# Performance work log

Measured on AMD Instinct MI355X. Metric: run time of the kernel, lower is better.

Reference implementation:

```python
import jax, jax.numpy as jnp
import numpy as np

N = 50000          # nodes
E = 800000         # edges (before self-loops)
IN_CH = 16
HID = 32
HEADS = 4
NEG_SLOPE = 0.2    # PyG GATConv default leaky_relu slope


def add_self_loops(edge_index, n):
    loops = jnp.arange(n, dtype=edge_index.dtype)
    return jnp.concatenate([edge_index, jnp.stack([loops, loops])], axis=1)


def gat_layer(x, edge_index, W, a_src, a_dst, bias, heads, out_ch, concat):
    """PyG-style GATConv: gather -> attention logits -> segment softmax over dst -> scatter."""
    n = x.shape[0]
    h = (x @ W).reshape(n, heads, out_ch)            # [N, H, C]
    src, dst = edge_index[0], edge_index[1]          # messages flow src -> dst
    alpha_src = (h * a_src).sum(-1)                  # [N, H]
    alpha_dst = (h * a_dst).sum(-1)                  # [N, H]
    e = jax.nn.leaky_relu(alpha_src[src] + alpha_dst[dst], NEG_SLOPE)  # [Etot, H]
    # numerically stable segment softmax over incoming edges of each dst node
    e_max = jax.ops.segment_max(e, dst, num_segments=n)
    e_exp = jnp.exp(e - e_max[dst])
    denom = jax.ops.segment_sum(e_exp, dst, num_segments=n)
    alpha = e_exp / (denom[dst] + 1e-16)             # [Etot, H]
    out = jax.ops.segment_sum(h[src] * alpha[..., None], dst, num_segments=n)  # [N, H, C]
    out = out.reshape(n, heads * out_ch) if concat else out.mean(axis=1)
    return out + bias


def setup_inputs() -> dict:
    key = jax.random.key(0)
    ks = jax.random.split(key, 10)
    x = jax.random.normal(ks[0], (N, IN_CH), dtype=jnp.float32)
    edge_index = jax.random.randint(ks[1], (2, E), 0, N, dtype=jnp.int64)
    s = 0.1
    W1 = jax.random.normal(ks[2], (IN_CH, HEADS * HID), dtype=jnp.float32) * s
    a_src1 = jax.random.normal(ks[3], (1, HEADS, HID), dtype=jnp.float32) * s
    a_dst1 = jax.random.normal(ks[4], (1, HEADS, HID), dtype=jnp.float32) * s
    b1 = jnp.zeros((HEADS * HID,), dtype=jnp.float32)
    W2 = jax.random.normal(ks[5], (HEADS * HID, 2), dtype=jnp.float32) * s
    a_src2 = jax.random.normal(ks[6], (1, 1, 2), dtype=jnp.float32) * s
    a_dst2 = jax.random.normal(ks[7], (1, 1, 2), dtype=jnp.float32) * s
    b2 = jnp.zeros((2,), dtype=jnp.float32)
    return {"x": x, "edge_index": edge_index,
            "W1": W1, "a_src1": a_src1, "a_dst1": a_dst1, "b1": b1,
            "W2": W2, "a_src2": a_src2, "a_dst2": a_dst2, "b2": b2}


def reference(x, edge_index, W1, a_src1, a_dst1, b1, W2, a_src2, a_dst2, b2):
    ei = add_self_loops(edge_index, x.shape[0])
    h = gat_layer(x, ei, W1, a_src1, a_dst1, b1, HEADS, HID, concat=True)
    h = jax.nn.relu(h)
    out = gat_layer(h, ei, W2, a_src2, a_dst2, b2, 1, 2, concat=False)
    return out
```

## Files before the change

kernel.cpp:

```cpp
#include <hip/hip_runtime.h>
#include <hip/hip_bf16.h>

#define N_NODES 50000
#define N_EDGES 800000
#define ETOT    (N_EDGES + N_NODES)
#define STRIDE  64
#define IN_CH   16
#define HID     32
#define HEADS   4
#define C1      (HEADS * HID)
#define NEG     0.2f

#define DEG_BLOCKS ((ETOT / 4 + 255) / 256)
#define NGROUPS    (N_NODES / 4)
#define H1_BLOCKS  2048

typedef unsigned short u16;
typedef unsigned int   u32;

__device__ __forceinline__ float bf2f(u16 b) {
    return __uint_as_float(((u32)b) << 16);
}

__device__ __forceinline__ u16 f2bf(float f) {
    __hip_bfloat16 hb = __float2bfloat16(f);
    return *(u16*)&hb;
}

__device__ __forceinline__ int clampn(int v) {
    return v < 0 ? 0 : (v >= N_NODES ? N_NODES - 1 : v);
}

__device__ __forceinline__ int eidx(const int* ei, int e, int i64, int which) {
    int v = i64 ? ei[2 * (which * N_EDGES + e)] : ei[which * N_EDGES + e];
    return clampn(v);
}

__device__ __forceinline__ float cvt(const void* src, int i, int bf) {
    return bf ? bf2f(((const u16*)src)[i]) : ((const float*)src)[i];
}

__device__ __forceinline__ int probe_bf_wave(const u16* xb) {
    int l = threadIdx.x & 63;
    int my = 0;
#pragma unroll
    for (int k = 0; k < 4; k++) {
        float f = bf2f(xb[l * 4 + k]);
        float a = fabsf(f);
        if (f == 0.0f || (a > 9.5e-7f && a < 1.05e6f)) my++;
    }
#pragma unroll
    for (int m = 32; m; m >>= 1) my += __shfl_xor(my, m);
    return my >= 224;
}

__device__ __forceinline__ int probe_i64_wave(const int* ei32) {
    int l = threadIdx.x & 63;
    int nz = (l < 32 && ei32[2 * l + 1] != 0) ? 1 : 0;
#pragma unroll
    for (int m = 32; m; m >>= 1) nz += __shfl_xor(nz, m);
    return nz == 0;
}

__device__ __forceinline__ void dev_deg(const int* __restrict__ ei,
                                        int* __restrict__ degs,
                                        u32* __restrict__ srp, int blk) {
    int i64 = probe_i64_wave(ei);
    int e0 = (blk * 256 + (int)threadIdx.x) * 4;
    if (e0 >= ETOT) return;
    int s[4], d[4];
#pragma unroll
    for (int j = 0; j < 4; j++) {
        int e = e0 + j;
        if (e < N_EDGES) { s[j] = eidx(ei, e, i64, 0); d[j] = eidx(ei, e, i64, 1); }
        else             { s[j] = d[j] = e - N_EDGES; }
    }
    u32 r[4];
#pragma unroll
    for (int j = 0; j < 4; j++) {
        u32 rr = (u32)atomicAdd(&degs[d[j]], 1) + 1u;
        r[j] = ((u32)s[j] << 16) | (rr > 0xFFFFu ? 0xFFFFu : rr);
    }
    *(uint4*)(srp + e0) = make_uint4(r[0], r[1], r[2], r[3]);
}

__device__ __forceinline__ void dev_fill(const int* __restrict__ ei,
                                         const u32* __restrict__ srp,
                                         u16* __restrict__ csr, int blk) {
    int i64 = probe_i64_wave(ei);
    int e0 = (blk * 256 + (int)threadIdx.x) * 4;
    if (e0 >= ETOT) return;
    uint4 q = *(const uint4*)(srp + e0);
    u32 sr[4] = {q.x, q.y, q.z, q.w};
#pragma unroll
    for (int j = 0; j < 4; j++) {
        int e = e0 + j;
        int d = (e < N_EDGES) ? eidx(ei, e, i64, 1) : (e - N_EDGES);
        u32 r = sr[j] & 0xFFFFu;
        if (r < STRIDE) csr[d * STRIDE + r] = (u16)(sr[j] >> 16);
    }
}

__device__ __forceinline__ void dev_h1(const void* __restrict__ x,
                                       const void* __restrict__ W1,
                                       const void* __restrict__ a_s,
                                       const void* __restrict__ a_d,
                                       u32* __restrict__ h1u,
                                       float* __restrict__ as1,
                                       float* __restrict__ ad1,
                                       float* Ws, float* As, float* Ad, int blk) {
    int bf = probe_bf_wave((const u16*)x);
    if (blk == 0 && threadIdx.x < 4) as1[N_NODES * 4 + threadIdx.x] = -1e30f;
    if (bf) {
        const u32* w32 = (const u32*)W1;
        for (int i = threadIdx.x; i < IN_CH * C1 / 2; i += 256) {
            u32 v = w32[i];
            Ws[2 * i]     = bf2f((u16)(v & 0xFFFF));
            Ws[2 * i + 1] = bf2f((u16)(v >> 16));
        }
        const u32* s32 = (const u32*)a_s;
        const u32* d32 = (const u32*)a_d;
        for (int i = threadIdx.x; i < C1 / 2; i += 256) {
            u32 vs = s32[i], vd = d32[i];
            As[2 * i]     = bf2f((u16)(vs & 0xFFFF));
            As[2 * i + 1] = bf2f((u16)(vs >> 16));
            Ad[2 * i]     = bf2f((u16)(vd & 0xFFFF));
            Ad[2 * i + 1] = bf2f((u16)(vd >> 16));
        }
    } else {
        for (int i = threadIdx.x; i < IN_CH * C1; i += 256) Ws[i] = ((const float*)W1)[i];
        for (int i = threadIdx.x; i < C1; i += 256) {
            As[i] = ((const float*)a_s)[i];
            Ad[i] = ((const float*)a_d)[i];
        }
    }
    __syncthreads();

    int w = threadIdx.x >> 6, l = threadIdx.x & 63;
    int c0 = 2 * l, c1 = 2 * l + 1;
    for (int g = blk; g < NGROUPS; g += H1_BLOCKS) {
        int n = g * 4 + w;
        float xval = (l < IN_CH) ? cvt(x, n * IN_CH + l, bf) : 0.f;
        float acc0 = 0.f, acc1 = 0.f;
#pragma unroll
        for (int k = 0; k < IN_CH; k++) {
            float xk = __shfl(xval, k);
            acc0 += xk * Ws[k * C1 + c0];
            acc1 += xk * Ws[k * C1 + c1];
        }
        h1u[n * 64 + l] = (u32)f2bf(acc0) | ((u32)f2bf(acc1) << 16);

        float ps = acc0 * As[c0] + acc1 * As[c1];
        float pd = acc0 * Ad[c0] + acc1 * Ad[c1];
#pragma unroll
        for (int m = 8; m; m >>= 1) { ps += __shfl_xor(ps, m); pd += __shfl_xor(pd, m); }
        if ((l & 15) == 0) {
            int hd = l >> 4;
            as1[n * 4 + hd] = ps;
            ad1[n * 4 + hd] = pd;
        }
    }
}

__launch_bounds__(256)
__global__ void k_deg_h1(const void* __restrict__ x, const int* __restrict__ ei,
                         const void* __restrict__ W1, const void* __restrict__ a_s,
                         const void* __restrict__ a_d,
                         int* __restrict__ degs, u32* __restrict__ srp,
                         u32* __restrict__ h1u, float* __restrict__ as1,
                         float* __restrict__ ad1) {
    __shared__ float Ws[IN_CH * C1];
    __shared__ float As[C1], Ad[C1];
    if (blockIdx.x < DEG_BLOCKS) { dev_deg(ei, degs, srp, blockIdx.x); return; }
    dev_h1(x, W1, a_s, a_d, h1u, as1, ad1, Ws, As, Ad, blockIdx.x - DEG_BLOCKS);
}

__launch_bounds__(256)
__global__ void k_deg(const int* __restrict__ ei, int* __restrict__ degs,
                      u32* __restrict__ srp) {
    dev_deg(ei, degs, srp, blockIdx.x);
}

__launch_bounds__(256)
__global__ void k_fill(const int* __restrict__ ei, const u32* __restrict__ srp,
                       u16* __restrict__ csr) {
    dev_fill(ei, srp, csr, blockIdx.x);
}

__launch_bounds__(256)
__global__ void k_h1_only(const void* __restrict__ x, const void* __restrict__ W1,
                          const void* __restrict__ a_s, const void* __restrict__ a_d,
                          u32* __restrict__ h1u, float* __restrict__ as1,
                          float* __restrict__ ad1) {
    __shared__ float Ws[IN_CH * C1];
    __shared__ float As[C1], Ad[C1];
    dev_h1(x, W1, a_s, a_d, h1u, as1, ad1, Ws, As, Ad, blockIdx.x);
}

__launch_bounds__(256)
__global__ void k_gather1(const void* __restrict__ x,
                          const int* __restrict__ degs, const u16* __restrict__ csr,
                          const u32* __restrict__ h1u,
                          const float* __restrict__ as1, const float* __restrict__ ad1,
                          const void* __restrict__ b1, const void* __restrict__ W2,
                          const void* __restrict__ a2s, const void* __restrict__ a2d,
                          float* __restrict__ h2, float* __restrict__ as2,
                          float* __restrict__ ad2) {
    int bf = probe_bf_wave((const u16*)x);
    int n = blockIdx.x * 4 + (threadIdx.x >> 6);
    int l = threadIdx.x & 63;
    int hd = l >> 4;
    int je = l & 7;
    int jh = (l >> 3) & 3;
    float advb = ad1[n * 4 + jh];
    int deg = degs[n] + 1;
    deg = deg > STRIDE ? STRIDE : deg;
    int nb = (deg + 7) >> 3;
    const u16* row = csr + (size_t)n * STRIDE;
    float acc0 = 0.f, acc1 = 0.f, swd = 0.f;

    int se = (int)row[je];
    if (se >= N_NODES) se = N_NODES;
    for (int b = 0; b < nb; b++) {
        int se_next = 0xFFFF;
        if (b + 1 < nb) se_next = (int)row[(b + 1) * 8 + je];
        float t = as1[se * 4 + jh] + advb;
        t = t > 0.f ? t : NEG * t;
        float wm = __expf(t);
        swd += wm;
#pragma unroll
        for (int j = 0; j < 8; j++) {
            int   sj = __shfl(se, j);
            float wj = __shfl(wm, hd * 8 + j);
            u32 p = h1u[sj * 64 + l];
            acc0 += wj * bf2f((u16)(p & 0xFFFF));
            acc1 += wj * bf2f((u16)(p >> 16));
        }
        se = se_next >= N_NODES ? N_NODES : se_next;
    }

    swd += __shfl_xor(swd, 1);
    swd += __shfl_xor(swd, 2);
    swd += __shfl_xor(swd, 4);
    float sw = __shfl(swd, hd * 8);

    float inv = 1.0f / sw;
    float v0 = acc0 * inv + cvt(b1, 2 * l, bf);
    float v1 = acc1 * inv + cvt(b1, 2 * l + 1, bf);
    v0 = v0 > 0.f ? v0 : 0.f;
    v1 = v1 > 0.f ? v1 : 0.f;
    float p0 = v0 * cvt(W2, 4 * l,     bf) + v1 * cvt(W2, 4 * l + 2, bf);
    float p1 = v0 * cvt(W2, 4 * l + 1, bf) + v1 * cvt(W2, 4 * l + 3, bf);
#pragma unroll
    for (int d = 32; d; d >>= 1) { p0 += __shfl_down(p0, d); p1 += __shfl_down(p1, d); }
    if (l == 0) {
        h2[n * 2] = p0; h2[n * 2 + 1] = p1;
        as2[n] = p0 * cvt(a2s, 0, bf) + p1 * cvt(a2s, 1, bf);
        ad2[n] = p0 * cvt(a2d, 0, bf) + p1 * cvt(a2d, 1, bf);
    }
}

__launch_bounds__(256)
__global__ void k_gather2(const void* __restrict__ x,
                          const int* __restrict__ degs, const u16* __restrict__ csr,
                          const float* __restrict__ h2, const float* __restrict__ as2,
                          const float* __restrict__ ad2, const void* __restrict__ b2,
                          void* __restrict__ out) {
    int bf = probe_bf_wave((const u16*)x);
    int n = blockIdx.x * 16 + (threadIdx.x >> 4);
    int g = threadIdx.x & 15;
    float adv = ad2[n], a0 = 0.f, a1 = 0.f, sw = 0.f;
    int deg = degs[n] + 1;
    deg = deg > STRIDE ? STRIDE : deg;
    const u16* row = csr + (size_t)n * STRIDE;
    for (int k = g; k < deg; k += 16) {
        int s = (int)row[k];
        float lg = as2[s] + adv;
        lg = lg > 0.f ? lg : NEG * lg;
        float w = __expf(lg);
        float2 hv = ((const float2*)h2)[s];
        a0 += w * hv.x;
        a1 += w * hv.y;
        sw += w;
    }
#pragma unroll
    for (int m = 8; m; m >>= 1) {
        a0 += __shfl_xor(a0, m); a1 += __shfl_xor(a1, m); sw += __shfl_xor(sw, m);
    }
    if (g == 0) {
        float inv = 1.0f / sw;
        float o0 = a0 * inv + cvt(b2, 0, bf);
        float o1 = a1 * inv + cvt(b2, 1, bf);
        if (bf) {
            ((u32*)out)[n] = (u32)f2bf(o0) | ((u32)f2bf(o1) << 16);
        } else {
            ((float2*)out)[n] = make_float2(o0, o1);
        }
    }
}

extern "C" void kernel_launch(void* const* d_in, const int* in_sizes, int n_in,
                              void* d_out, int out_size, void* d_ws, size_t ws_size,
                              hipStream_t stream) {
    const void* x    = d_in[0];
    const int*  ei   = (const int*)d_in[1];
    const void* W1   = d_in[2];
    const void* a_s1 = d_in[3];
    const void* a_d1 = d_in[4];
    const void* b1   = d_in[5];
    const void* W2   = d_in[6];
    const void* a_s2 = d_in[7];
    const void* a_d2 = d_in[8];
    const void* b2   = d_in[9];

    char* p = (char*)d_ws;
    int*   degs = (int*)p;     p += ((size_t)N_NODES * 4 + 255) & ~255;
    u16*   csr  = (u16*)p;     p += (size_t)N_NODES * STRIDE * 2;
    size_t init_bytes = (size_t)(p - (char*)d_ws);
    u32*   h1u  = (u32*)p;     p += (size_t)(N_NODES + 1) * 64 * 4;
    float* as1  = (float*)p;   p += (size_t)(N_NODES + 1) * HEADS * 4;
    float* ad1  = (float*)p;   p += (size_t)N_NODES * HEADS * 4;
    float* h2   = (float*)p;   p += (size_t)N_NODES * 2 * 4;
    float* as2  = (float*)p;   p += (size_t)N_NODES * 4;
    float* ad2  = (float*)p;   p += (size_t)N_NODES * 4;
    size_t base_used = (size_t)(p - (char*)d_ws);
    size_t srp_bytes = (size_t)ETOT * 4;

    hipMemsetAsync(degs, 0xFF, init_bytes, stream);

    if (ws_size >= base_used + srp_bytes) {
        u32* srp = (u32*)p;
        k_deg_h1<<<DEG_BLOCKS + H1_BLOCKS, 256, 0, stream>>>(
            x, ei, W1, a_s1, a_d1, degs, srp, h1u, as1, ad1);
        k_fill<<<DEG_BLOCKS, 256, 0, stream>>>(ei, srp, csr);
    } else {
        u32* srp = h1u;
        k_deg<<<DEG_BLOCKS, 256, 0, stream>>>(ei, degs, srp);
        k_fill<<<DEG_BLOCKS, 256, 0, stream>>>(ei, srp, csr);
        k_h1_only<<<H1_BLOCKS, 256, 0, stream>>>(x, W1, a_s1, a_d1, h1u, as1, ad1);
    }
    k_gather1<<<N_NODES / 4, 256, 0, stream>>>(
        x, degs, csr, h1u, as1, ad1, b1, W2, a_s2, a_d2, h2, as2, ad2);
    k_gather2<<<N_NODES / 16, 256, 0, stream>>>(
        x, degs, csr, h2, as2, ad2, b2, d_out);
}
```

Baseline: 204.2 us.

## Fuse degree count and CSR fill, keep layer-1 weights in registers

Merges the degree-counting and CSR-fill passes into one. Each edge's atomicAdd return value now writes the source index straight into its slot of the padded CSR, which removes the intermediate srp buffer, one kernel launch and a second read of edge_index. The h1 projection now loads W1 and the attention vectors into per-lane registers and reads each node's x row with vector loads. That drops the shared-memory staging, the __syncthreads and the per-k shuffles, at the cost of higher register use. The workspace-size fallback path is removed, and the padding row of h1u is zeroed explicitly.

```diff
diff --git a/kernel.cpp b/kernel.cpp
--- a/kernel.cpp
+++ b/kernel.cpp
@@ -62,9 +62,9 @@
     return nz == 0;
 }
 
-__device__ __forceinline__ void dev_deg(const int* __restrict__ ei,
-                                        int* __restrict__ degs,
-                                        u32* __restrict__ srp, int blk) {
+__device__ __forceinline__ void dev_degfill(const int* __restrict__ ei,
+                                            int* __restrict__ degs,
+                                            u16* __restrict__ csr, int blk) {
     int i64 = probe_i64_wave(ei);
     int e0 = (blk * 256 + (int)threadIdx.x) * 4;
     if (e0 >= ETOT) return;
@@ -75,29 +75,10 @@
         if (e < N_EDGES) { s[j] = eidx(ei, e, i64, 0); d[j] = eidx(ei, e, i64, 1); }
         else             { s[j] = d[j] = e - N_EDGES; }
     }
-    u32 r[4];
 #pragma unroll
     for (int j = 0; j < 4; j++) {
-        u32 rr = (u32)atomicAdd(&degs[d[j]], 1) + 1u;
-        r[j] = ((u32)s[j] << 16) | (rr > 0xFFFFu ? 0xFFFFu : rr);
-    }
-    *(uint4*)(srp + e0) = make_uint4(r[0], r[1], r[2], r[3]);
-}
-
-__device__ __forceinline__ void dev_fill(const int* __restrict__ ei,
-                                         const u32* __restrict__ srp,
-                                         u16* __restrict__ csr, int blk) {
-    int i64 = probe_i64_wave(ei);
-    int e0 = (blk * 256 + (int)threadIdx.x) * 4;
-    if (e0 >= ETOT) return;
-    uint4 q = *(const uint4*)(srp + e0);
-    u32 sr[4] = {q.x, q.y, q.z, q.w};
-#pragma unroll
-    for (int j = 0; j < 4; j++) {
-        int e = e0 + j;
-        int d = (e < N_EDGES) ? eidx(ei, e, i64, 1) : (e - N_EDGES);
-        u32 r = sr[j] & 0xFFFFu;
-        if (r < STRIDE) csr[d * STRIDE + r] = (u16)(sr[j] >> 16);
+        u32 r = (u32)atomicAdd(&degs[d[j]], 1) + 1u;
+        if (r < STRIDE) csr[(size_t)d[j] * STRIDE + r] = (u16)s[j];
     }
 }
 
@@ -107,51 +88,72 @@
                                        const void* __restrict__ a_d,
                                        u32* __restrict__ h1u,
                                        float* __restrict__ as1,
-                                       float* __restrict__ ad1,
-                                       float* Ws, float* As, float* Ad, int blk) {
+                                       float* __restrict__ ad1, int blk) {
     int bf = probe_bf_wave((const u16*)x);
     if (blk == 0 && threadIdx.x < 4) as1[N_NODES * 4 + threadIdx.x] = -1e30f;
+    if (blk == 0 && threadIdx.x >= 64 && threadIdx.x < 128)
+        h1u[N_NODES * 64 + (threadIdx.x - 64)] = 0;
+
+    int w = threadIdx.x >> 6, l = threadIdx.x & 63;
+
+    float wa[IN_CH], wb[IN_CH];
     if (bf) {
         const u32* w32 = (const u32*)W1;
-        for (int i = threadIdx.x; i < IN_CH * C1 / 2; i += 256) {
-            u32 v = w32[i];
-            Ws[2 * i]     = bf2f((u16)(v & 0xFFFF));
-            Ws[2 * i + 1] = bf2f((u16)(v >> 16));
-        }
-        const u32* s32 = (const u32*)a_s;
-        const u32* d32 = (const u32*)a_d;
-        for (int i = threadIdx.x; i < C1 / 2; i += 256) {
-            u32 vs = s32[i], vd = d32[i];
-            As[2 * i]     = bf2f((u16)(vs & 0xFFFF));
-            As[2 * i + 1] = bf2f((u16)(vs >> 16));
-            Ad[2 * i]     = bf2f((u16)(vd & 0xFFFF));
-            Ad[2 * i + 1] = bf2f((u16)(vd >> 16));
+#pragma unroll
+        for (int k = 0; k < IN_CH; k++) {
+            u32 v = w32[k * 64 + l];
+            wa[k] = bf2f((u16)(v & 0xFFFF));
+            wb[k] = bf2f((u16)(v >> 16));
         }
     } else {
-        for (int i = threadIdx.x; i < IN_CH * C1; i += 256) Ws[i] = ((const float*)W1)[i];
-        for (int i = threadIdx.x; i < C1; i += 256) {
-            As[i] = ((const float*)a_s)[i];
-            Ad[i] = ((const float*)a_d)[i];
-        }
-    }
-    __syncthreads();
-
-    int w = threadIdx.x >> 6, l = threadIdx.x & 63;
-    int c0 = 2 * l, c1 = 2 * l + 1;
+        const float2* w64 = (const float2*)W1;
+#pragma unroll
+        for (int k = 0; k < IN_CH; k++) {
+            float2 v = w64[k * 64 + l];
+            wa[k] = v.x; wb[k] = v.y;
+        }
+    }
+    float asa, asb, ada, adb;
+    if (bf) {
+        u32 vs = ((const u32*)a_s)[l], vd = ((const u32*)a_d)[l];
+        asa = bf2f((u16)(vs & 0xFFFF)); asb = bf2f((u16)(vs >> 16));
+        ada = bf2f((u16)(vd & 0xFFFF)); adb = bf2f((u16)(vd >> 16));
+    } else {
+        float2 vs = ((const float2*)a_s)[l], vd = ((const float2*)a_d)[l];
+        asa = vs.x; asb = vs.y; ada = vd.x; adb = vd.y;
+    }
+
     for (int g = blk; g < NGROUPS; g += H1_BLOCKS) {
         int n = g * 4 + w;
-        float xval = (l < IN_CH) ? cvt(x, n * IN_CH + l, bf) : 0.f;
+        float xr[IN_CH];
+        if (bf) {
+            const uint4* xp = (const uint4*)((const u16*)x + (size_t)n * IN_CH);
+            uint4 q0 = xp[0], q1 = xp[1];
+            u32 qq[8] = {q0.x, q0.y, q0.z, q0.w, q1.x, q1.y, q1.z, q1.w};
+#pragma unroll
+            for (int k = 0; k < 8; k++) {
+                xr[2 * k]     = bf2f((u16)(qq[k] & 0xFFFF));
+                xr[2 * k + 1] = bf2f((u16)(qq[k] >> 16));
+            }
+        } else {
+            const float4* xp = (const float4*)((const float*)x + (size_t)n * IN_CH);
+#pragma unroll
+            for (int k = 0; k < 4; k++) {
+                float4 q = xp[k];
+                xr[4 * k] = q.x; xr[4 * k + 1] = q.y;
+                xr[4 * k + 2] = q.z; xr[4 * k + 3] = q.w;
+            }
+        }
         float acc0 = 0.f, acc1 = 0.f;
 #pragma unroll
         for (int k = 0; k < IN_CH; k++) {
-            float xk = __shfl(xval, k);
-            acc0 += xk * Ws[k * C1 + c0];
-            acc1 += xk * Ws[k * C1 + c1];
+            acc0 += xr[k] * wa[k];
+            acc1 += xr[k] * wb[k];
         }
         h1u[n * 64 + l] = (u32)f2bf(acc0) | ((u32)f2bf(acc1) << 16);
 
-        float ps = acc0 * As[c0] + acc1 * As[c1];
-        float pd = acc0 * Ad[c0] + acc1 * Ad[c1];
+        float ps = acc0 * asa + acc1 * asb;
+        float pd = acc0 * ada + acc1 * adb;
 #pragma unroll
         for (int m = 8; m; m >>= 1) { ps += __shfl_xor(ps, m); pd += __shfl_xor(pd, m); }
         if ((l & 15) == 0) {
@@ -166,35 +168,11 @@
 __global__ void k_deg_h1(const void* __restrict__ x, const int* __restrict__ ei,
                          const void* __restrict__ W1, const void* __restrict__ a_s,
                          const void* __restrict__ a_d,
-                         int* __restrict__ degs, u32* __restrict__ srp,
+                         int* __restrict__ degs, u16* __restrict__ csr,
                          u32* __restrict__ h1u, float* __restrict__ as1,
                          float* __restrict__ ad1) {
-    __shared__ float Ws[IN_CH * C1];
-    __shared__ float As[C1], Ad[C1];
-    if (blockIdx.x < DEG_BLOCKS) { dev_deg(ei, degs, srp, blockIdx.x); return; }
-    dev_h1(x, W1, a_s, a_d, h1u, as1, ad1, Ws, As, Ad, blockIdx.x - DEG_BLOCKS);
-}
-
-__launch_bounds__(256)
-__global__ void k_deg(const int* __restrict__ ei, int* __restrict__ degs,
-                      u32* __restrict__ srp) {
-    dev_deg(ei, degs, srp, blockIdx.x);
-}
-
-__launch_bounds__(256)
-__global__ void k_fill(const int* __restrict__ ei, const u32* __restrict__ srp,
-                       u16* __restrict__ csr) {
-    dev_fill(ei, srp, csr, blockIdx.x);
-}
-
-__launch_bounds__(256)
-__global__ void k_h1_only(const void* __restrict__ x, const void* __restrict__ W1,
-                          const void* __restrict__ a_s, const void* __restrict__ a_d,
-                          u32* __restrict__ h1u, float* __restrict__ as1,
-                          float* __restrict__ ad1) {
-    __shared__ float Ws[IN_CH * C1];
-    __shared__ float As[C1], Ad[C1];
-    dev_h1(x, W1, a_s, a_d, h1u, as1, ad1, Ws, As, Ad, blockIdx.x);
+    if (blockIdx.x < DEG_BLOCKS) { dev_degfill(ei, degs, csr, blockIdx.x); return; }
+    dev_h1(x, W1, a_s, a_d, h1u, as1, ad1, blockIdx.x - DEG_BLOCKS);
 }
 
 __launch_bounds__(256)
@@ -323,22 +301,11 @@
     float* h2   = (float*)p;   p += (size_t)N_NODES * 2 * 4;
     float* as2  = (float*)p;   p += (size_t)N_NODES * 4;
     float* ad2  = (float*)p;   p += (size_t)N_NODES * 4;
-    size_t base_used = (size_t)(p - (char*)d_ws);
-    size_t srp_bytes = (size_t)ETOT * 4;
 
     hipMemsetAsync(degs, 0xFF, init_bytes, stream);
 
-    if (ws_size >= base_used + srp_bytes) {
-        u32* srp = (u32*)p;
-        k_deg_h1<<<DEG_BLOCKS + H1_BLOCKS, 256, 0, stream>>>(
-            x, ei, W1, a_s1, a_d1, degs, srp, h1u, as1, ad1);
-        k_fill<<<DEG_BLOCKS, 256, 0, stream>>>(ei, srp, csr);
-    } else {
-        u32* srp = h1u;
-        k_deg<<<DEG_BLOCKS, 256, 0, stream>>>(ei, degs, srp);
-        k_fill<<<DEG_BLOCKS, 256, 0, stream>>>(ei, srp, csr);
-        k_h1_only<<<H1_BLOCKS, 256, 0, stream>>>(x, W1, a_s1, a_d1, h1u, as1, ad1);
-    }
+    k_deg_h1<<<DEG_BLOCKS + H1_BLOCKS, 256, 0, stream>>>(
+        x, ei, W1, a_s1, a_d1, degs, csr, h1u, as1, ad1);
     k_gather1<<<N_NODES / 4, 256, 0, stream>>>(
         x, degs, csr, h1u, as1, ad1, b1, W2, a_s2, a_d2, h2, as2, ad2);
     k_gather2<<<N_NODES / 16, 256, 0, stream>>>(
```

Measured after the change: 211.3 us. +3.5%, slower.
